# Kernel tuning notes

Measured on AMD Instinct MI355X. Metric: run time of the kernel, lower is better.

Reference implementation:

```python
import jax, jax.numpy as jnp
import numpy as np

N_NODES, T, C_IN, B = 207, 12, 4, 4
NT = N_NODES * T
D, H = 96, 4
HD = D // H
FF = 4 * D
ENC_L, DEC_L = 4, 1
N_MASK = int(NT * 0.75)
N_UNMASK = NT - N_MASK
MAX_NEIGH = 40
ATTN_SCALE = 1.0 / float(np.sqrt(HD))
SQRT_D = float(np.sqrt(D))


def _ln(x, g, b, eps=1e-5):
    m = jnp.mean(x, -1, keepdims=True)
    v = jnp.mean((x - m) ** 2, -1, keepdims=True)
    return (x - m) * jax.lax.rsqrt(v + eps) * g + b


def _transformer(x, attn_mask, layers):
    # x: [B, S, D]; attn_mask: [S, S] bool (True = disallowed) or None.
    x = x * SQRT_D  # nn.Transformer-style input scaling
    def step(h, p):
        aw, ab, W1, B1, W2, B2, LN = p
        Bq, S, _ = h.shape
        q = (h @ aw[0] + ab[0]).reshape(Bq, S, H, HD)
        k = (h @ aw[1] + ab[1]).reshape(Bq, S, H, HD)
        v = (h @ aw[2] + ab[2]).reshape(Bq, S, H, HD)
        scores = jnp.einsum('bqhd,bkhd->bhqk', q, k) * ATTN_SCALE
        if attn_mask is not None:
            scores = jnp.where(attn_mask, jnp.float32(-1e30), scores)
        probs = jax.nn.softmax(scores, axis=-1)
        o = jnp.einsum('bhqk,bkhd->bqhd', probs, v).reshape(Bq, S, D)
        h = _ln(h + o @ aw[3] + ab[3], LN[0, 0], LN[0, 1])  # post-norm (torch default)
        f = jax.nn.relu(h @ W1 + B1) @ W2 + B2
        h = _ln(h + f, LN[1, 0], LN[1, 1])
        return h, None
    x, _ = jax.lax.scan(step, x, layers)
    return x


def _layer_params(key, nlayers):
    ks = jax.random.split(key, 3)
    attn_w = jax.random.normal(ks[0], (nlayers, 4, D, D), jnp.float32) / float(np.sqrt(D))
    w1 = jax.random.normal(ks[1], (nlayers, D, FF), jnp.float32) / float(np.sqrt(D))
    w2 = jax.random.normal(ks[2], (nlayers, FF, D), jnp.float32) / float(np.sqrt(FF))
    ln = jnp.broadcast_to(jnp.stack([jnp.ones(D), jnp.zeros(D)]), (nlayers, 2, 2, D)).astype(jnp.float32)
    return (attn_w, jnp.zeros((nlayers, 4, D), jnp.float32), w1,
            jnp.zeros((nlayers, FF), jnp.float32), w2, jnp.zeros((nlayers, D), jnp.float32), ln)


def setup_inputs() -> dict:
    key = jax.random.key(0)
    ks = jax.random.split(key, 12)
    rng = np.random.default_rng(42)
    perm = rng.permutation(NT)
    masked_idx = jnp.asarray(np.sort(perm[:N_MASK]), jnp.int32)
    unmasked_idx = jnp.asarray(np.sort(perm[N_MASK:]), jnp.int32)
    ea = _layer_params(ks[3], ENC_L)
    da = _layer_params(ks[4], DEC_L)
    return dict(
        history_data=jax.random.uniform(ks[0], (B, T, N_NODES, C_IN), jnp.float32),
        unmasked_idx=unmasked_idx, masked_idx=masked_idx,
        nodevec1=jax.random.normal(ks[1], (N_NODES, 10), jnp.float32),
        nodevec2=jax.random.normal(ks[2], (10, N_NODES), jnp.float32),
        dim_w=jax.random.normal(ks[5], (1, D), jnp.float32),
        dim_b=jnp.zeros((D,), jnp.float32),
        pos_emb=jax.random.uniform(ks[6], (NT, D), jnp.float32, -0.02, 0.02),
        tod_w=jax.random.normal(ks[7], (1, D), jnp.float32) * 0.02,
        tod_b=jnp.zeros((D,), jnp.float32),
        dow_w=jax.random.normal(ks[8], (1, D), jnp.float32) * 0.02,
        dow_b=jnp.zeros((D,), jnp.float32),
        mask_token=jax.random.normal(ks[9], (D,), jnp.float32) * 0.02,
        enc_attn_w=ea[0], enc_attn_b=ea[1], enc_ffn_w1=ea[2], enc_ffn_b1=ea[3],
        enc_ffn_w2=ea[4], enc_ffn_b2=ea[5], enc_ln=ea[6],
        enc_norm_g=jnp.ones((D,), jnp.float32), enc_norm_b=jnp.zeros((D,), jnp.float32),
        e2d_w=jax.random.normal(ks[10], (D, D), jnp.float32) / float(np.sqrt(D)),
        e2d_b=jnp.zeros((D,), jnp.float32),
        dec_attn_w=da[0], dec_attn_b=da[1], dec_ffn_w1=da[2], dec_ffn_b1=da[3],
        dec_ffn_w2=da[4], dec_ffn_b2=da[5], dec_ln=da[6],
        dec_norm_g=jnp.ones((D,), jnp.float32), dec_norm_b=jnp.zeros((D,), jnp.float32),
        out_w=jax.random.normal(ks[11], (D, 1), jnp.float32) / float(np.sqrt(D)),
        out_b=jnp.zeros((1,), jnp.float32),
    )


def reference(history_data, unmasked_idx, masked_idx, nodevec1, nodevec2,
              dim_w, dim_b, pos_emb, tod_w, tod_b, dow_w, dow_b, mask_token,
              enc_attn_w, enc_attn_b, enc_ffn_w1, enc_ffn_b1, enc_ffn_w2, enc_ffn_b2, enc_ln,
              enc_norm_g, enc_norm_b, e2d_w, e2d_b,
              dec_attn_w, dec_attn_b, dec_ffn_w1, dec_ffn_b1, dec_ffn_w2, dec_ffn_b2, dec_ln,
              dec_norm_g, dec_norm_b, out_w, out_b):
    hist = jnp.transpose(history_data, (0, 2, 3, 1))  # [B, N, C, T]
    tod = hist[:, :, 3:4, :].reshape(B, NT, 1)
    dow = hist[:, :, 2:3, :].reshape(B, NT, 1)
    # --- adaptive graph: softmax(relu(v1 v2)), threshold + top-40, straight-through ---
    A = jax.nn.softmax(jax.nn.relu(nodevec1 @ nodevec2), axis=1)
    kth = -jnp.sort(-A, axis=1)[:, MAX_NEIGH:MAX_NEIGH + 1]  # (MAX_NEIGH+1)-th largest per row
    keep = jnp.logical_and(A > 1.0 / N_NODES, A > kth).astype(A.dtype)
    bin_mask = jax.lax.stop_gradient(keep - A) + A
    adpA = A * bin_mask
    adpA_full = jnp.repeat(jnp.repeat(adpA, T, axis=0), T, axis=1)  # [NT, NT] block structure
    # --- embed + positional/temporal encoding ---
    x = jnp.transpose(hist[:, :, 0:1, :], (0, 1, 3, 2)) @ dim_w + dim_b  # [B, N, T, D]
    token = x.reshape(B, NT, D) + pos_emb + (tod @ tod_w + tod_b) + (dow @ dow_w + dow_b)
    # --- encoder over unmasked tokens with graph-derived attention mask ---
    enc_in = token[:, unmasked_idx, :]
    A_sub = adpA_full[unmasked_idx][:, unmasked_idx]
    attn_mask = A_sub == 0  # ~A.bool(): True = disallowed
    h = _transformer(enc_in, attn_mask,
                     (enc_attn_w, enc_attn_b, enc_ffn_w1, enc_ffn_b1, enc_ffn_w2, enc_ffn_b2, enc_ln))
    h = _ln(h, enc_norm_g, enc_norm_b)
    # --- decoder ---
    h = h @ e2d_w + e2d_b
    h_masked = (mask_token[None, None, :] + pos_emb[masked_idx]
                + (tod[:, masked_idx] @ tod_w + tod_b)
                + (dow[:, masked_idx] @ dow_w + dow_b))  # [B, N_MASK, D]
    full = jnp.concatenate([h, h_masked], axis=1)  # [B, NT, D]
    full = _transformer(full, None,
                        (dec_attn_w, dec_attn_b, dec_ffn_w1, dec_ffn_b1, dec_ffn_w2, dec_ffn_b2, dec_ln))
    full = _ln(full, dec_norm_g, dec_norm_b)
    recon = full @ out_w + out_b  # [B, NT, 1]
    recon_masked = recon[:, N_UNMASK:, :]
    label = jnp.transpose(hist, (0, 1, 3, 2))[:, :, :, 0].reshape(B, NT, 1)
    label_masked = label[:, masked_idx, :]
    return recon_masked, label_masked
```

## Files before the change

### kernel.cpp

```cpp
#include <hip/hip_runtime.h>
#include <math.h>

#define N_NODES 207
#define T_STEPS 12
#define NT 2484
#define BQ 4
#define DIM 96
#define NH 4
#define HD 24
#define FFD 384
#define N_MASK 1863
#define N_UNMASK 621
#define MAX_NEIGH 40
#define ATTN_SCALE 0.20412414523193154f
#define SQRT_DF 9.797958971132712f
#define KT 256
#define NMW 20

static inline int cdiv(int a, int b) { return (a + b - 1) / b; }

__global__ __launch_bounds__(256) void adj_kernel(const float* __restrict__ nv1,
                                                  const float* __restrict__ nv2,
                                                  float* __restrict__ keep) {
    int r = blockIdx.x, t = threadIdx.x;
    __shared__ float a[N_NODES];
    __shared__ float red[256];
    __shared__ int   redi[256];
    __shared__ int   taken[N_NODES];
    __shared__ float v1[10];
    __shared__ float kth;
    if (t < 10) v1[t] = nv1[r * 10 + t];
    __syncthreads();
    if (t < N_NODES) {
        float s = 0.f;
#pragma unroll
        for (int c = 0; c < 10; ++c) s += v1[c] * nv2[c * N_NODES + t];
        a[t] = fmaxf(s, 0.f);
        taken[t] = 0;
    }
    __syncthreads();
    red[t] = (t < N_NODES) ? a[t] : -3e38f;
    __syncthreads();
    for (int s = 128; s > 0; s >>= 1) {
        if (t < s) red[t] = fmaxf(red[t], red[t + s]);
        __syncthreads();
    }
    float mx = red[0];
    __syncthreads();
    float e = 0.f;
    if (t < N_NODES) e = __expf(a[t] - mx);
    red[t] = e;
    __syncthreads();
    for (int s = 128; s > 0; s >>= 1) {
        if (t < s) red[t] += red[t + s];
        __syncthreads();
    }
    float inv = 1.f / red[0];
    __syncthreads();
    if (t < N_NODES) a[t] = e * inv;
    __syncthreads();
    for (int round = 0; round <= MAX_NEIGH; ++round) {
        red[t]  = (t < N_NODES && !taken[t]) ? a[t] : -1.f;
        redi[t] = t;
        __syncthreads();
        for (int s = 128; s > 0; s >>= 1) {
            if (t < s && red[t + s] > red[t]) { red[t] = red[t + s]; redi[t] = redi[t + s]; }
            __syncthreads();
        }
        if (t == 0) {
            taken[redi[0]] = 1;
            if (round == MAX_NEIGH) kth = red[0];
        }
        __syncthreads();
    }
    if (t < N_NODES) {
        float av = a[t];
        keep[r * N_NODES + t] = (av > (1.f / 207.f) && av > kth) ? 1.f : 0.f;
    }
}

__global__ void unnode_kernel(const int* __restrict__ uidx, int* __restrict__ unn) {
    int i = blockIdx.x * blockDim.x + threadIdx.x;
    if (i < N_UNMASK) unn[i] = uidx[i] / T_STEPS;
}

__global__ void maskbits_kernel(const float* __restrict__ keep, const int* __restrict__ unn,
                                unsigned int* __restrict__ mw) {
    int q = blockIdx.x;
    int w = threadIdx.x;
    if (w >= NMW) return;
    const float* krow = keep + unn[q] * N_NODES;
    unsigned int word = 0;
    for (int j = 0; j < 32; ++j) {
        int k = w * 32 + j;
        if (k < N_UNMASK && krow[unn[k]] != 0.f) word |= (1u << j);
    }
    mw[q * NMW + w] = word;
}

__global__ void encin_kernel(const float* __restrict__ hist, const int* __restrict__ uidx,
                             const float* __restrict__ dim_w, const float* __restrict__ dim_b,
                             const float* __restrict__ pos,
                             const float* __restrict__ tod_w, const float* __restrict__ tod_b,
                             const float* __restrict__ dow_w, const float* __restrict__ dow_b,
                             float* __restrict__ h) {
    int idx = blockIdx.x * blockDim.x + threadIdx.x;
    if (idx >= BQ * N_UNMASK * DIM) return;
    int d = idx % DIM;
    int q = (idx / DIM) % N_UNMASK;
    int b = idx / (DIM * N_UNMASK);
    int u = uidx[q];
    int n = u / T_STEPS, t = u % T_STEPS;
    const float* hp = hist + ((size_t)(b * T_STEPS + t) * N_NODES + n) * 4;
    float h0 = hp[0], dw = hp[2], td = hp[3];
    float val = h0 * dim_w[d] + dim_b[d] + pos[u * DIM + d]
              + td * tod_w[d] + tod_b[d] + dw * dow_w[d] + dow_b[d];
    h[idx] = val * SQRT_DF;
}

__global__ void hmasked_kernel(const float* __restrict__ hist, const int* __restrict__ midx,
                               const float* __restrict__ mask_token, const float* __restrict__ pos,
                               const float* __restrict__ tod_w, const float* __restrict__ tod_b,
                               const float* __restrict__ dow_w, const float* __restrict__ dow_b,
                               float* __restrict__ full) {
    int idx = blockIdx.x * blockDim.x + threadIdx.x;
    if (idx >= BQ * N_MASK * DIM) return;
    int d = idx % DIM;
    int j = (idx / DIM) % N_MASK;
    int b = idx / (DIM * N_MASK);
    int m = midx[j];
    int n = m / T_STEPS, t = m % T_STEPS;
    const float* hp = hist + ((size_t)(b * T_STEPS + t) * N_NODES + n) * 4;
    float dw = hp[2], td = hp[3];
    float val = mask_token[d] + pos[m * DIM + d]
              + td * tod_w[d] + tod_b[d] + dw * dow_w[d] + dow_b[d];
    full[((size_t)(b * NT) + N_UNMASK + j) * DIM + d] = val * SQRT_DF;
}

__global__ void label_kernel(const float* __restrict__ hist, const int* __restrict__ midx,
                             float* __restrict__ out) {
    int idx = blockIdx.x * blockDim.x + threadIdx.x;
    if (idx >= BQ * N_MASK) return;
    int j = idx % N_MASK;
    int b = idx / N_MASK;
    int m = midx[j];
    int n = m / T_STEPS, t = m % T_STEPS;
    out[BQ * N_MASK + idx] = hist[((size_t)(b * T_STEPS + t) * N_NODES + n) * 4 + 0];
}

#define ACCROW(accv, av)                                          \
    accv.x += av.x*w0.x + av.y*w1.x + av.z*w2.x + av.w*w3.x;      \
    accv.y += av.x*w0.y + av.y*w1.y + av.z*w2.y + av.w*w3.y;      \
    accv.z += av.x*w0.z + av.y*w1.z + av.z*w2.z + av.w*w3.z;      \
    accv.w += av.x*w0.w + av.y*w1.w + av.z*w2.w + av.w*w3.w;

template<int WMODE>
__global__ __launch_bounds__(256) void tgemm_kernel(const float* __restrict__ A,
                                                    const float* __restrict__ W,
                                                    const float* __restrict__ bias,
                                                    const float* __restrict__ res,
                                                    float* __restrict__ C,
                                                    int M, int N, int K, int gm,
                                                    int relu, float scale, int rmode) {
    __shared__ float As[64][100];
    __shared__ float Ws[96][64];
    int tid = threadIdx.x;
    int bm = blockIdx.x % gm;
    int bn = blockIdx.x / gm;
    int m0 = bm * 64, n0 = bn * 64;
    int tn4 = (tid & 15) * 4;
    int tm4 = (tid >> 4) * 4;
    float4 acc0 = {0,0,0,0}, acc1 = {0,0,0,0}, acc2 = {0,0,0,0}, acc3 = {0,0,0,0};

    for (int kc = 0; kc < K; kc += 96) {
        if (kc) __syncthreads();
#pragma unroll
        for (int i = 0; i < 6; ++i) {
            int f = i * 256 + tid;
            int r = f / 24, c4 = (f % 24) * 4;
            float4 v = {0,0,0,0};
            if (m0 + r < M) v = *(const float4*)(A + (size_t)(m0 + r) * K + kc + c4);
            *(float4*)&As[r][c4] = v;
        }
#pragma unroll
        for (int i = 0; i < 6; ++i) {
            int f = i * 256 + tid;
            int kr = f >> 4, n4 = (f & 15) * 4;
            int gn = n0 + n4;
            float4 v = {0,0,0,0};
            if (gn < N) {
                if (WMODE == 0) {
                    v = *(const float4*)(W + (size_t)(kc + kr) * N + gn);
                } else {
                    int gg = gn / 96, nc = gn - gg * 96;
                    v = *(const float4*)(W + (size_t)gg * 9216 + (kc + kr) * 96 + nc);
                }
            }
            *(float4*)&Ws[kr][n4] = v;
        }
        __syncthreads();
#pragma unroll 4
        for (int k = 0; k < 96; k += 4) {
            float4 a0 = *(const float4*)&As[tm4 + 0][k];
            float4 a1 = *(const float4*)&As[tm4 + 1][k];
            float4 a2 = *(const float4*)&As[tm4 + 2][k];
            float4 a3 = *(const float4*)&As[tm4 + 3][k];
            float4 w0 = *(const float4*)&Ws[k + 0][tn4];
            float4 w1 = *(const float4*)&Ws[k + 1][tn4];
            float4 w2 = *(const float4*)&Ws[k + 2][tn4];
            float4 w3 = *(const float4*)&Ws[k + 3][tn4];
            ACCROW(acc0, a0)
            ACCROW(acc1, a1)
            ACCROW(acc2, a2)
            ACCROW(acc3, a3)
        }
    }

    int gn = n0 + tn4;
    if (gn >= N) return;
    float4 bv = *(const float4*)(bias + gn);
    float4 av[4] = {acc0, acc1, acc2, acc3};
#pragma unroll
    for (int i = 0; i < 4; ++i) {
        int grow = m0 + tm4 + i;
        if (grow >= M) break;
        float4 acc = av[i];
        acc.x += bv.x; acc.y += bv.y; acc.z += bv.z; acc.w += bv.w;
        if (res) {
            int rr = grow;
            if (rmode) { int bb = grow / N_MASK; rr = bb * NT + N_UNMASK + (grow - bb * N_MASK); }
            float4 rv = *(const float4*)(res + (size_t)rr * N + gn);
            acc.x += rv.x; acc.y += rv.y; acc.z += rv.z; acc.w += rv.w;
        }
        if (relu) {
            acc.x = fmaxf(acc.x, 0.f); acc.y = fmaxf(acc.y, 0.f);
            acc.z = fmaxf(acc.z, 0.f); acc.w = fmaxf(acc.w, 0.f);
        }
        acc.x *= scale; acc.y *= scale; acc.z *= scale; acc.w *= scale;
        *(float4*)(C + (size_t)grow * N + gn) = acc;
    }
}

template<int QPL>
__global__ __launch_bounds__(256) void fattn_kernel(const float* __restrict__ Qp,
                                                    const float* __restrict__ Kp,
                                                    const float* __restrict__ Vp,
                                                    float* __restrict__ Pm,
                                                    float* __restrict__ Pl,
                                                    float* __restrict__ Pacc,
                                                    const unsigned int* __restrict__ maskw,
                                                    int S, int Sq, int qoff,
                                                    int nqt, int NS, int rs) {
    __shared__ float smem[12288];
    float* Ks = smem;
    float* Vs = smem + 6144;

    int t = threadIdx.x;
    int w = t >> 6, lane = t & 63;
    int bid = blockIdx.x;
    int ns = bid % NS; int r1 = bid / NS;
    int qt = r1 % nqt; r1 /= nqt;
    int hh = r1 % NH;
    int b  = r1 / NH;

    float qr[QPL][HD];
    bool qvalid[QPL];
#pragma unroll
    for (int h = 0; h < QPL; ++h) {
        int qidx = qt * (64 * QPL) + h * 64 + lane;
        qvalid[h] = qidx < Sq;
        if (qvalid[h]) {
            const float* qp = Qp + ((size_t)(b * S + qoff + qidx)) * rs + hh * HD;
#pragma unroll
            for (int i = 0; i < 6; ++i) {
                float4 v = *(const float4*)(qp + i * 4);
                qr[h][i*4+0] = v.x; qr[h][i*4+1] = v.y;
                qr[h][i*4+2] = v.z; qr[h][i*4+3] = v.w;
            }
        } else {
#pragma unroll
            for (int d = 0; d < HD; ++d) qr[h][d] = 0.f;
        }
    }

    float m[QPL], l[QPL];
    float acc[QPL][HD];
#pragma unroll
    for (int h = 0; h < QPL; ++h) {
        m[h] = -1e30f; l[h] = 0.f;
#pragma unroll
        for (int d = 0; d < HD; ++d) acc[h][d] = 0.f;
    }

    int ntile = (S + KT - 1) / KT;
    int tpn = (ntile + NS - 1) / NS;
    int c0 = ns * tpn;
    int c1 = min(c0 + tpn, ntile);

    for (int c = c0; c < c1; ++c) {
        __syncthreads();
        int base_k = c * KT;
#pragma unroll
        for (int i = 0; i < 6; ++i) {
            int fi = i * 256 + t;
            int row = fi / 6, cc = fi - row * 6;
            int gk = base_k + row;
            float4 kv = {0,0,0,0};
            float4 vv = {0,0,0,0};
            if (gk < S) {
                size_t roff = ((size_t)(b * S + gk)) * rs + hh * HD + cc * 4;
                kv = *(const float4*)(Kp + roff);
                vv = *(const float4*)(Vp + roff);
            }
            *(float4*)(Ks + row * HD + cc * 4) = kv;
            *(float4*)(Vs + row * HD + cc * 4) = vv;
        }
        __syncthreads();

        unsigned int mw0 = ~0u, mw1 = ~0u;
        if (QPL == 1 && maskw) {
            int qidx = qt * 64 + lane;
            if (qidx < Sq) {
                int wi = c * 8 + w * 2;
                mw0 = (wi     < NMW) ? maskw[qidx * NMW + wi]     : 0u;
                mw1 = (wi + 1 < NMW) ? maskw[qidx * NMW + wi + 1] : 0u;
            }
        }

        for (int g = 0; g < 16; ++g) {
            float sgrp[QPL][4];
            float pv[QPL][4];
#pragma unroll
            for (int j = 0; j < 4; ++j) {
                int j2 = g * 4 + j;
                int kk = (w << 6) + j2;
                int gk = base_k + kk;
                const float4* kr = (const float4*)(Ks + kk * HD);
                float d0[QPL];
#pragma unroll
                for (int h = 0; h < QPL; ++h) d0[h] = 0.f;
#pragma unroll
                for (int i = 0; i < 6; ++i) {
                    float4 kv = kr[i];
#pragma unroll
                    for (int h = 0; h < QPL; ++h) {
                        d0[h] += qr[h][i*4+0]*kv.x + qr[h][i*4+1]*kv.y
                               + qr[h][i*4+2]*kv.z + qr[h][i*4+3]*kv.w;
                    }
                }
#pragma unroll
                for (int h = 0; h < QPL; ++h) {
                    float s = d0[h] * ATTN_SCALE;
                    if (QPL == 1 && maskw) {
                        unsigned int wsel = (j2 & 32) ? mw1 : mw0;
                        if (!((wsel >> (j2 & 31)) & 1u)) s = -1e30f;
                    }
                    if (gk >= S) s = -INFINITY;
                    sgrp[h][j] = s;
                }
            }
#pragma unroll
            for (int h = 0; h < QPL; ++h) {
                float gmx = fmaxf(fmaxf(sgrp[h][0], sgrp[h][1]),
                                  fmaxf(sgrp[h][2], sgrp[h][3]));
                if (gmx > m[h]) {
                    float f = __expf(m[h] - gmx);
                    l[h] *= f;
#pragma unroll
                    for (int d = 0; d < HD; ++d) acc[h][d] *= f;
                    m[h] = gmx;
                }
#pragma unroll
                for (int j = 0; j < 4; ++j) {
                    float p = __expf(sgrp[h][j] - m[h]);
                    pv[h][j] = p;
                    l[h] += p;
                }
            }
#pragma unroll
            for (int j = 0; j < 4; ++j) {
                int kk = (w << 6) + g * 4 + j;
                const float4* vr = (const float4*)(Vs + kk * HD);
#pragma unroll
                for (int i = 0; i < 6; ++i) {
                    float4 vv = vr[i];
#pragma unroll
                    for (int h = 0; h < QPL; ++h) {
                        acc[h][i*4+0] += pv[h][j]*vv.x;
                        acc[h][i*4+1] += pv[h][j]*vv.y;
                        acc[h][i*4+2] += pv[h][j]*vv.z;
                        acc[h][i*4+3] += pv[h][j]*vv.w;
                    }
                }
            }
        }
    }

#pragma unroll
    for (int h = 0; h < QPL; ++h) {
        __syncthreads();
        float* my = smem + (size_t)(w * 64 + lane) * 27;
        my[0] = m[h]; my[1] = l[h];
#pragma unroll
        for (int d = 0; d < HD; ++d) my[2 + d] = acc[h][d];
        __syncthreads();
        if (t < 64) {
            int qidx = qt * (64 * QPL) + h * 64 + t;
            if (qidx < Sq) {
                float M2 = -INFINITY;
#pragma unroll
                for (int w2 = 0; w2 < 4; ++w2)
                    M2 = fmaxf(M2, smem[(size_t)(w2 * 64 + t) * 27]);
                float L = 0.f;
                float o[HD];
#pragma unroll
                for (int d = 0; d < HD; ++d) o[d] = 0.f;
#pragma unroll
                for (int w2 = 0; w2 < 4; ++w2) {
                    const float* pp = smem + (size_t)(w2 * 64 + t) * 27;
                    float f = __expf(pp[0] - M2);
                    L += pp[1] * f;
#pragma unroll
                    for (int d = 0; d < HD; ++d) o[d] += pp[2 + d] * f;
                }
                size_t pb = ((size_t)((b * NH + hh) * NS + ns)) * Sq + qidx;
                Pm[pb] = M2;
                Pl[pb] = L;
                float* pa = Pacc + pb * 24;
#pragma unroll
                for (int i = 0; i < 6; ++i)
                    *(float4*)(pa + i * 4) = make_float4(o[i*4+0], o[i*4+1],
                                                         o[i*4+2], o[i*4+3]);
            }
        }
    }
}

__global__ __launch_bounds__(256) void attn_combine_kernel(const float* __restrict__ Pm,
                                                           const float* __restrict__ Pl,
                                                           const float* __restrict__ Pacc,
                                                           float* __restrict__ O,
                                                           int Sq, int NS) {
    int tid = blockIdx.x * 256 + threadIdx.x;
    if (tid >= BQ * NH * Sq * 6) return;
    int d4 = tid % 6;
    int q  = (tid / 6) % Sq;
    int bh = tid / (6 * Sq);
    float M = -1e30f;
    for (int ns = 0; ns < NS; ++ns)
        M = fmaxf(M, Pm[((size_t)bh * NS + ns) * Sq + q]);
    float L = 0.f;
    float ax = 0.f, ay = 0.f, az = 0.f, aw = 0.f;
    for (int ns = 0; ns < NS; ++ns) {
        size_t pb = ((size_t)bh * NS + ns) * Sq + q;
        float wgt = __expf(Pm[pb] - M);
        L += wgt * Pl[pb];
        float4 f0 = *(const float4*)(Pacc + pb * 24 + d4 * 4);
        ax += wgt * f0.x; ay += wgt * f0.y;
        az += wgt * f0.z; aw += wgt * f0.w;
    }
    float inv = 1.f / L;
    int b = bh >> 2, hh = bh & 3;
    float* op = O + ((size_t)(b * Sq + q)) * DIM + hh * HD + d4 * 4;
    *(float4*)op = make_float4(ax * inv, ay * inv, az * inv, aw * inv);
}

__global__ __launch_bounds__(256) void ln_kernel(const float* __restrict__ X,
                                                 const float* __restrict__ g,
                                                 const float* __restrict__ bta,
                                                 float* __restrict__ Y, int M) {
    int row = blockIdx.x * 4 + (threadIdx.x >> 6);
    if (row >= M) return;
    int lane = threadIdx.x & 63;
    const float* x = X + (size_t)row * DIM;
    float x0 = x[lane];
    float x1 = (lane < 32) ? x[64 + lane] : 0.f;
    float s = x0 + x1;
#pragma unroll
    for (int o = 32; o; o >>= 1) s += __shfl_xor(s, o);
    float mean = s * (1.f / DIM);
    float d0 = x0 - mean;
    float d1 = (lane < 32) ? (x1 - mean) : 0.f;
    float v = d0 * d0 + d1 * d1;
#pragma unroll
    for (int o = 32; o; o >>= 1) v += __shfl_xor(v, o);
    float rs = rsqrtf(v * (1.f / DIM) + 1e-5f);
    float* y = Y + (size_t)row * DIM;
    y[lane] = d0 * rs * g[lane] + bta[lane];
    if (lane < 32) y[64 + lane] = d1 * rs * g[64 + lane] + bta[64 + lane];
}

__global__ __launch_bounds__(256) void tail_kernel(const float* __restrict__ X,
                                                   const float* __restrict__ g1,
                                                   const float* __restrict__ b1,
                                                   const float* __restrict__ g2,
                                                   const float* __restrict__ b2,
                                                   const float* __restrict__ ow,
                                                   const float* __restrict__ ob,
                                                   float* __restrict__ out, int Mtail) {
    int row = blockIdx.x * 4 + (threadIdx.x >> 6);
    if (row >= Mtail) return;
    int lane = threadIdx.x & 63;
    bool lo = lane < 32;
    const float* x = X + (size_t)row * DIM;
    float x0 = x[lane];
    float x1 = lo ? x[64 + lane] : 0.f;
    float s = x0 + x1;
#pragma unroll
    for (int o = 32; o; o >>= 1) s += __shfl_xor(s, o);
    float mean = s * (1.f / DIM);
    float d0 = x0 - mean;
    float d1 = lo ? (x1 - mean) : 0.f;
    float v = d0 * d0 + d1 * d1;
#pragma unroll
    for (int o = 32; o; o >>= 1) v += __shfl_xor(v, o);
    float rs = rsqrtf(v * (1.f / DIM) + 1e-5f);
    float y0 = d0 * rs * g1[lane] + b1[lane];
    float y1 = lo ? (d1 * rs * g1[64 + lane] + b1[64 + lane]) : 0.f;
    s = y0 + y1;
#pragma unroll
    for (int o = 32; o; o >>= 1) s += __shfl_xor(s, o);
    mean = s * (1.f / DIM);
    d0 = y0 - mean;
    d1 = lo ? (y1 - mean) : 0.f;
    v = d0 * d0 + d1 * d1;
#pragma unroll
    for (int o = 32; o; o >>= 1) v += __shfl_xor(v, o);
    rs = rsqrtf(v * (1.f / DIM) + 1e-5f);
    float z0 = d0 * rs * g2[lane] + b2[lane];
    float z1 = lo ? (d1 * rs * g2[64 + lane] + b2[64 + lane]) : 0.f;
    float a = z0 * ow[lane] + (lo ? z1 * ow[64 + lane] : 0.f);
#pragma unroll
    for (int o = 32; o; o >>= 1) a += __shfl_xor(a, o);
    if (lane == 0) out[row] = a + ob[0];
}

__global__ void copy_enc_kernel(const float* __restrict__ src, float* __restrict__ full) {
    int idx = blockIdx.x * blockDim.x + threadIdx.x;
    if (idx >= BQ * N_UNMASK * DIM) return;
    int d = idx % DIM;
    int q = (idx / DIM) % N_UNMASK;
    int b = idx / (DIM * N_UNMASK);
    full[((size_t)(b * NT) + q) * DIM + d] = src[idx];
}

extern "C" void kernel_launch(void* const* d_in, const int* in_sizes, int n_in,
                              void* d_out, int out_size, void* d_ws, size_t ws_size,
                              hipStream_t stream) {
    const float* hist   = (const float*)d_in[0];
    const int*   uidx   = (const int*)d_in[1];
    const int*   midx   = (const int*)d_in[2];
    const float* nv1    = (const float*)d_in[3];
    const float* nv2    = (const float*)d_in[4];
    const float* dim_w  = (const float*)d_in[5];
    const float* dim_b  = (const float*)d_in[6];
    const float* pos    = (const float*)d_in[7];
    const float* tod_w  = (const float*)d_in[8];
    const float* tod_b  = (const float*)d_in[9];
    const float* dow_w  = (const float*)d_in[10];
    const float* dow_b  = (const float*)d_in[11];
    const float* mtok   = (const float*)d_in[12];
    const float* eaw    = (const float*)d_in[13];
    const float* eab    = (const float*)d_in[14];
    const float* ew1    = (const float*)d_in[15];
    const float* eb1    = (const float*)d_in[16];
    const float* ew2    = (const float*)d_in[17];
    const float* eb2    = (const float*)d_in[18];
    const float* eln    = (const float*)d_in[19];
    const float* eng    = (const float*)d_in[20];
    const float* enb    = (const float*)d_in[21];
    const float* e2dw   = (const float*)d_in[22];
    const float* e2db   = (const float*)d_in[23];
    const float* daw    = (const float*)d_in[24];
    const float* dab    = (const float*)d_in[25];
    const float* dw1    = (const float*)d_in[26];
    const float* db1    = (const float*)d_in[27];
    const float* dw2    = (const float*)d_in[28];
    const float* db2    = (const float*)d_in[29];
    const float* dln    = (const float*)d_in[30];
    const float* dng    = (const float*)d_in[31];
    const float* dnb    = (const float*)d_in[32];
    const float* ow     = (const float*)d_in[33];
    const float* ob     = (const float*)d_in[34];

    float* ws = (float*)d_ws;
    float*        keep  = ws;
    int*          unn   = (int*)(ws + 43008);
    unsigned int* maskw = (unsigned int*)(ws + 44032);
    float* eh = ws + 56576;
    float* e1 = ws + 295040;
    float* e2 = ws + 1248896;
    float* et = ws + 1487360;
    float* fh = ws + 1725824;
    float* qf = ws + 2679680;
    float* dh = ws + 5541248;
    float* dt = ws + 6256640;
    float* PaccE = ws + 5541248;
    float* PmE   = ws + 6256640;
    float* PlE   = ws + 6286448;
    float* PaccD = ws + 56576;
    float* PmD   = ws + 1487360;
    float* PlD   = ws + 1546976;
    float* dLN = e1;

    float* outp = (float*)d_out;
    const int ME = BQ * N_UNMASK;
    const int MD = BQ * NT;
    const int MT = BQ * N_MASK;
    const int gmE = cdiv(ME, 64);
    const int gmD = cdiv(MD, 64);
    const int gmT = cdiv(MT, 64);
    const int NSE = 3, NSD = 2;
    const int nqtE = 10;
    const int nqtD = 15;

    adj_kernel<<<N_NODES, 256, 0, stream>>>(nv1, nv2, keep);
    unnode_kernel<<<cdiv(N_UNMASK, 256), 256, 0, stream>>>(uidx, unn);
    maskbits_kernel<<<N_UNMASK, 32, 0, stream>>>(keep, unn, maskw);
    encin_kernel<<<cdiv(ME * DIM, 256), 256, 0, stream>>>(
        hist, uidx, dim_w, dim_b, pos, tod_w, tod_b, dow_w, dow_b, eh);
    label_kernel<<<cdiv(MT, 256), 256, 0, stream>>>(hist, midx, outp);

    for (int l = 0; l < 4; ++l) {
        const float* aw = eaw + (size_t)l * 4 * DIM * DIM;
        const float* ab = eab + (size_t)l * 4 * DIM;
        tgemm_kernel<1><<<gmE * 5, 256, 0, stream>>>(
            eh, aw, ab, nullptr, e1, ME, 288, 96, gmE, 0, 1.f, 0);
        fattn_kernel<1><<<BQ * NH * nqtE * NSE, 256, 0, stream>>>(
            e1, e1 + 96, e1 + 192, PmE, PlE, PaccE, maskw,
            N_UNMASK, N_UNMASK, 0, nqtE, NSE, 288);
        attn_combine_kernel<<<cdiv(BQ * NH * N_UNMASK * 6, 256), 256, 0, stream>>>(
            PmE, PlE, PaccE, e2, N_UNMASK, NSE);
        tgemm_kernel<0><<<gmE * 2, 256, 0, stream>>>(
            e2, aw + 3 * DIM * DIM, ab + 3 * DIM, eh, et, ME, 96, 96, gmE, 0, 1.f, 0);
        ln_kernel<<<cdiv(ME, 4), 256, 0, stream>>>(
            et, eln + (size_t)(l * 4 + 0) * DIM, eln + (size_t)(l * 4 + 1) * DIM, eh, ME);
        tgemm_kernel<0><<<gmE * 6, 256, 0, stream>>>(
            eh, ew1 + (size_t)l * DIM * FFD, eb1 + (size_t)l * FFD, nullptr, e1,
            ME, FFD, 96, gmE, 1, 1.f, 0);
        tgemm_kernel<0><<<gmE * 2, 256, 0, stream>>>(
            e1, ew2 + (size_t)l * FFD * DIM, eb2 + (size_t)l * DIM, eh, et,
            ME, 96, FFD, gmE, 0, 1.f, 0);
        ln_kernel<<<cdiv(ME, 4), 256, 0, stream>>>(
            et, eln + (size_t)(l * 4 + 2) * DIM, eln + (size_t)(l * 4 + 3) * DIM, eh, ME);
    }
    ln_kernel<<<cdiv(ME, 4), 256, 0, stream>>>(eh, eng, enb, e2, ME);
    tgemm_kernel<0><<<gmE * 2, 256, 0, stream>>>(
        e2, e2dw, e2db, nullptr, et, ME, 96, 96, gmE, 0, SQRT_DF, 0);
    copy_enc_kernel<<<cdiv(ME * DIM, 256), 256, 0, stream>>>(et, fh);
    hmasked_kernel<<<cdiv(MT * DIM, 256), 256, 0, stream>>>(
        hist, midx, mtok, pos, tod_w, tod_b, dow_w, dow_b, fh);

    tgemm_kernel<1><<<gmD * 5, 256, 0, stream>>>(
        fh, daw, dab, nullptr, qf, MD, 288, 96, gmD, 0, 1.f, 0);
    fattn_kernel<2><<<BQ * NH * nqtD * NSD, 256, 0, stream>>>(
        qf, qf + 96, qf + 192, PmD, PlD, PaccD, nullptr,
        NT, N_MASK, N_UNMASK, nqtD, NSD, 288);
    attn_combine_kernel<<<cdiv(BQ * NH * N_MASK * 6, 256), 256, 0, stream>>>(
        PmD, PlD, PaccD, dh, N_MASK, NSD);
    tgemm_kernel<0><<<gmT * 2, 256, 0, stream>>>(
        dh, daw + 3 * DIM * DIM, dab + 3 * DIM, fh, dt, MT, 96, 96, gmT, 0, 1.f, 1);
    ln_kernel<<<cdiv(MT, 4), 256, 0, stream>>>(dt, dln + 0 * DIM, dln + 1 * DIM, dLN, MT);
    tgemm_kernel<0><<<gmT * 6, 256, 0, stream>>>(
        dLN, dw1, db1, nullptr, qf, MT, FFD, 96, gmT, 1, 1.f, 0);
    tgemm_kernel<0><<<gmT * 2, 256, 0, stream>>>(
        qf, dw2, db2, dLN, dh, MT, 96, FFD, gmT, 0, 1.f, 0);
    tail_kernel<<<cdiv(MT, 4), 256, 0, stream>>>(
        dh, dln + 2 * DIM, dln + 3 * DIM, dng, dnb, ow, ob, outp, MT);
}
```

Before: 700.4 us.

## Fuse residual add and LayerNorm into full-width N=96 GEMM epilogue

Adds a GEMM kernel where each block computes a 64-row tile across all 96 output columns, so the residual add and post-norm LayerNorm can run in the epilogue via 16-lane shuffle reductions. This replaces the separate out-projection/FFN2 GEMM plus ln_kernel launches in the encoder and decoder, and writes the encoder-to-decoder projection straight into the decoder buffer, which removes copy_enc_kernel. The tail kernel drops its first LayerNorm because that work now happens in the fused epilogue. The cost is fewer blocks per launch, one per 64 rows instead of two or more, which lowers parallelism on these small M sizes, and a larger shared-memory footprint per block.

```diff
diff --git a/kernel.cpp b/kernel.cpp
--- a/kernel.cpp
+++ b/kernel.cpp
@@ -238,6 +238,118 @@
         }
         acc.x *= scale; acc.y *= scale; acc.z *= scale; acc.w *= scale;
         *(float4*)(C + (size_t)grow * N + gn) = acc;
+    }
+}
+
+template<int DOLN>
+__global__ __launch_bounds__(256) void tgemm96_kernel(const float* __restrict__ A,
+                                                      const float* __restrict__ W,
+                                                      const float* __restrict__ bias,
+                                                      const float* __restrict__ res,
+                                                      const float* __restrict__ lng,
+                                                      const float* __restrict__ lnb,
+                                                      float* __restrict__ C,
+                                                      int M, int K,
+                                                      float scale, int rmode, int omode) {
+    __shared__ float As[64][100];
+    __shared__ float Ws[96][100];
+    int tid = threadIdx.x;
+    int m0 = blockIdx.x * 64;
+    int tc = tid & 15;
+    int tr = tid >> 4;
+    int colBase = tc * 6;
+    float acc[4][6];
+#pragma unroll
+    for (int r = 0; r < 4; ++r)
+#pragma unroll
+        for (int c = 0; c < 6; ++c) acc[r][c] = 0.f;
+
+    for (int kc = 0; kc < K; kc += 96) {
+        if (kc) __syncthreads();
+#pragma unroll
+        for (int i = 0; i < 6; ++i) {
+            int f = i * 256 + tid;
+            int r = f / 24, c4 = (f % 24) * 4;
+            float4 v = {0,0,0,0};
+            if (m0 + r < M) v = *(const float4*)(A + (size_t)(m0 + r) * K + kc + c4);
+            *(float4*)&As[r][c4] = v;
+        }
+#pragma unroll
+        for (int i = 0; i < 9; ++i) {
+            int f = i * 256 + tid;
+            int kr = f / 24, c4 = (f % 24) * 4;
+            float4 v = *(const float4*)(W + (size_t)(kc + kr) * 96 + c4);
+            *(float4*)&Ws[kr][c4] = v;
+        }
+        __syncthreads();
+#pragma unroll 4
+        for (int k = 0; k < 96; k += 4) {
+            float4 a0 = *(const float4*)&As[tr * 4 + 0][k];
+            float4 a1 = *(const float4*)&As[tr * 4 + 1][k];
+            float4 a2 = *(const float4*)&As[tr * 4 + 2][k];
+            float4 a3 = *(const float4*)&As[tr * 4 + 3][k];
+#pragma unroll
+            for (int i = 0; i < 4; ++i) {
+                float2 w01 = *(const float2*)&Ws[k + i][colBase];
+                float2 w23 = *(const float2*)&Ws[k + i][colBase + 2];
+                float2 w45 = *(const float2*)&Ws[k + i][colBase + 4];
+                float wv[6] = {w01.x, w01.y, w23.x, w23.y, w45.x, w45.y};
+                float ai[4] = { (i==0?a0.x:(i==1?a0.y:(i==2?a0.z:a0.w))),
+                                (i==0?a1.x:(i==1?a1.y:(i==2?a1.z:a1.w))),
+                                (i==0?a2.x:(i==1?a2.y:(i==2?a2.z:a2.w))),
+                                (i==0?a3.x:(i==1?a3.y:(i==2?a3.z:a3.w))) };
+#pragma unroll
+                for (int r = 0; r < 4; ++r)
+#pragma unroll
+                    for (int c = 0; c < 6; ++c)
+                        acc[r][c] += ai[r] * wv[c];
+            }
+        }
+    }
+
+    float bv[6];
+#pragma unroll
+    for (int c = 0; c < 6; ++c) bv[c] = bias[colBase + c];
+
+#pragma unroll
+    for (int r = 0; r < 4; ++r) {
+        int grow = m0 + tr * 4 + r;
+        bool valid = grow < M;
+        float v[6];
+#pragma unroll
+        for (int c = 0; c < 6; ++c) v[c] = acc[r][c] + bv[c];
+        if (res && valid) {
+            int rr = grow;
+            if (rmode) { int bb = grow / N_MASK; rr = bb * NT + N_UNMASK + (grow - bb * N_MASK); }
+            const float* rp = res + (size_t)rr * 96 + colBase;
+#pragma unroll
+            for (int c = 0; c < 6; ++c) v[c] += rp[c];
+        }
+#pragma unroll
+        for (int c = 0; c < 6; ++c) v[c] *= scale;
+        if (DOLN) {
+            float s = ((v[0] + v[1]) + (v[2] + v[3])) + (v[4] + v[5]);
+#pragma unroll
+            for (int o = 1; o <= 8; o <<= 1) s += __shfl_xor(s, o);
+            float mean = s * (1.f / 96.f);
+            float var = 0.f;
+#pragma unroll
+            for (int c = 0; c < 6; ++c) { float d = v[c] - mean; var += d * d; }
+#pragma unroll
+            for (int o = 1; o <= 8; o <<= 1) var += __shfl_xor(var, o);
+            float rs = rsqrtf(var * (1.f / 96.f) + 1e-5f);
+#pragma unroll
+            for (int c = 0; c < 6; ++c)
+                v[c] = (v[c] - mean) * rs * lng[colBase + c] + lnb[colBase + c];
+        }
+        if (valid) {
+            int orow = grow;
+            if (omode) { int bb = grow / N_UNMASK; orow = bb * NT + (grow - bb * N_UNMASK); }
+            float* cp = C + (size_t)orow * 96 + colBase;
+            *(float2*)(cp)     = make_float2(v[0], v[1]);
+            *(float2*)(cp + 2) = make_float2(v[2], v[3]);
+            *(float2*)(cp + 4) = make_float2(v[4], v[5]);
+        }
     }
 }
 
@@ -491,8 +603,6 @@
 }
 
 __global__ __launch_bounds__(256) void tail_kernel(const float* __restrict__ X,
-                                                   const float* __restrict__ g1,
-                                                   const float* __restrict__ b1,
                                                    const float* __restrict__ g2,
                                                    const float* __restrict__ b2,
                                                    const float* __restrict__ ow,
@@ -503,45 +613,24 @@
     int lane = threadIdx.x & 63;
     bool lo = lane < 32;
     const float* x = X + (size_t)row * DIM;
-    float x0 = x[lane];
-    float x1 = lo ? x[64 + lane] : 0.f;
-    float s = x0 + x1;
+    float y0 = x[lane];
+    float y1 = lo ? x[64 + lane] : 0.f;
+    float s = y0 + y1;
 #pragma unroll
     for (int o = 32; o; o >>= 1) s += __shfl_xor(s, o);
     float mean = s * (1.f / DIM);
-    float d0 = x0 - mean;
-    float d1 = lo ? (x1 - mean) : 0.f;
+    float d0 = y0 - mean;
+    float d1 = lo ? (y1 - mean) : 0.f;
     float v = d0 * d0 + d1 * d1;
 #pragma unroll
     for (int o = 32; o; o >>= 1) v += __shfl_xor(v, o);
     float rs = rsqrtf(v * (1.f / DIM) + 1e-5f);
-    float y0 = d0 * rs * g1[lane] + b1[lane];
-    float y1 = lo ? (d1 * rs * g1[64 + lane] + b1[64 + lane]) : 0.f;
-    s = y0 + y1;
-#pragma unroll
-    for (int o = 32; o; o >>= 1) s += __shfl_xor(s, o);
-    mean = s * (1.f / DIM);
-    d0 = y0 - mean;
-    d1 = lo ? (y1 - mean) : 0.f;
-    v = d0 * d0 + d1 * d1;
-#pragma unroll
-    for (int o = 32; o; o >>= 1) v += __shfl_xor(v, o);
-    rs = rsqrtf(v * (1.f / DIM) + 1e-5f);
     float z0 = d0 * rs * g2[lane] + b2[lane];
     float z1 = lo ? (d1 * rs * g2[64 + lane] + b2[64 + lane]) : 0.f;
     float a = z0 * ow[lane] + (lo ? z1 * ow[64 + lane] : 0.f);
 #pragma unroll
     for (int o = 32; o; o >>= 1) a += __shfl_xor(a, o);
     if (lane == 0) out[row] = a + ob[0];
-}
-
-__global__ void copy_enc_kernel(const float* __restrict__ src, float* __restrict__ full) {
-    int idx = blockIdx.x * blockDim.x + threadIdx.x;
-    if (idx >= BQ * N_UNMASK * DIM) return;
-    int d = idx % DIM;
-    int q = (idx / DIM) % N_UNMASK;
-    int b = idx / (DIM * N_UNMASK);
-    full[((size_t)(b * NT) + q) * DIM + d] = src[idx];
 }
 
 extern "C" void kernel_launch(void* const* d_in, const int* in_sizes, int n_in,
@@ -590,7 +679,6 @@
     float* eh = ws + 56576;
     float* e1 = ws + 295040;
     float* e2 = ws + 1248896;
-    float* et = ws + 1487360;
     float* fh = ws + 1725824;
     float* qf = ws + 2679680;
     float* dh = ws + 5541248;
@@ -601,7 +689,6 @@
     float* PaccD = ws + 56576;
     float* PmD   = ws + 1487360;
     float* PlD   = ws + 1546976;
-    float* dLN = e1;
 
     float* outp = (float*)d_out;
     const int ME = BQ * N_UNMASK;
@@ -631,23 +718,21 @@
             N_UNMASK, N_UNMASK, 0, nqtE, NSE, 288);
         attn_combine_kernel<<<cdiv(BQ * NH * N_UNMASK * 6, 256), 256, 0, stream>>>(
             PmE, PlE, PaccE, e2, N_UNMASK, NSE);
-        tgemm_kernel<0><<<gmE * 2, 256, 0, stream>>>(
-            e2, aw + 3 * DIM * DIM, ab + 3 * DIM, eh, et, ME, 96, 96, gmE, 0, 1.f, 0);
-        ln_kernel<<<cdiv(ME, 4), 256, 0, stream>>>(
-            et, eln + (size_t)(l * 4 + 0) * DIM, eln + (size_t)(l * 4 + 1) * DIM, eh, ME);
+        tgemm96_kernel<1><<<gmE, 256, 0, stream>>>(
+            e2, aw + 3 * DIM * DIM, ab + 3 * DIM, eh,
+            eln + (size_t)(l * 4 + 0) * DIM, eln + (size_t)(l * 4 + 1) * DIM,
+            eh, ME, 96, 1.f, 0, 0);
         tgemm_kernel<0><<<gmE * 6, 256, 0, stream>>>(
             eh, ew1 + (size_t)l * DIM * FFD, eb1 + (size_t)l * FFD, nullptr, e1,
             ME, FFD, 96, gmE, 1, 1.f, 0);
-        tgemm_kernel<0><<<gmE * 2, 256, 0, stream>>>(
-            e1, ew2 + (size_t)l * FFD * DIM, eb2 + (size_t)l * DIM, eh, et,
-            ME, 96, FFD, gmE, 0, 1.f, 0);
-        ln_kernel<<<cdiv(ME, 4), 256, 0, stream>>>(
-            et, eln + (size_t)(l * 4 + 2) * DIM, eln + (size_t)(l * 4 + 3) * DIM, eh, ME);
+        tgemm96_kernel<1><<<gmE, 256, 0, stream>>>(
+            e1, ew2 + (size_t)l * FFD * DIM, eb2 + (size_t)l * DIM, eh,
+            eln + (size_t)(l * 4 + 2) * DIM, eln + (size_t)(l * 4 + 3) * DIM,
+            eh, ME, FFD, 1.f, 0, 0);
     }
     ln_kernel<<<cdiv(ME, 4), 256, 0, stream>>>(eh, eng, enb, e2, ME);
-    tgemm_kernel<0><<<gmE * 2, 256, 0, stream>>>(
-        e2, e2dw, e2db, nullptr, et, ME, 96, 96, gmE, 0, SQRT_DF, 0);
-    copy_enc_kernel<<<cdiv(ME * DIM, 256), 256, 0, stream>>>(et, fh);
+    tgemm96_kernel<0><<<gmE, 256, 0, stream>>>(
+        e2, e2dw, e2db, nullptr, nullptr, nullptr, fh, ME, 96, SQRT_DF, 0, 1);
     hmasked_kernel<<<cdiv(MT * DIM, 256), 256, 0, stream>>>(
         hist, midx, mtok, pos, tod_w, tod_b, dow_w, dow_b, fh);
 
@@ -658,13 +743,13 @@
         NT, N_MASK, N_UNMASK, nqtD, NSD, 288);
     attn_combine_kernel<<<cdiv(BQ * NH * N_MASK * 6, 256), 256, 0, stream>>>(
         PmD, PlD, PaccD, dh, N_MASK, NSD);
-    tgemm_kernel<0><<<gmT * 2, 256, 0, stream>>>(
-        dh, daw + 3 * DIM * DIM, dab + 3 * DIM, fh, dt, MT, 96, 96, gmT, 0, 1.f, 1);
-    ln_kernel<<<cdiv(MT, 4), 256, 0, stream>>>(dt, dln + 0 * DIM, dln + 1 * DIM, dLN, MT);
+    tgemm96_kernel<1><<<gmT, 256, 0, stream>>>(
+        dh, daw + 3 * DIM * DIM, dab + 3 * DIM, fh,
+        dln + 0 * DIM, dln + 1 * DIM, dt, MT, 96, 1.f, 1, 0);
     tgemm_kernel<0><<<gmT * 6, 256, 0, stream>>>(
-        dLN, dw1, db1, nullptr, qf, MT, FFD, 96, gmT, 1, 1.f, 0);
-    tgemm_kernel<0><<<gmT * 2, 256, 0, stream>>>(
-        qf, dw2, db2, dLN, dh, MT, 96, FFD, gmT, 0, 1.f, 0);
+        dt, dw1, db1, nullptr, qf, MT, FFD, 96, gmT, 1, 1.f, 0);
+    tgemm96_kernel<1><<<gmT, 256, 0, stream>>>(
+        qf, dw2, db2, dt, dln + 2 * DIM, dln + 3 * DIM, dh, MT, FFD, 1.f, 0, 0);
     tail_kernel<<<cdiv(MT, 4), 256, 0, stream>>>(
-        dh, dln + 2 * DIM, dln + 3 * DIM, dng, dnb, ow, ob, outp, MT);
-}
+        dh, dng, dnb, ow, ob, outp, MT);
+}
```

Measured after the change: 715.1 us. 1.02x slower.

## Fuse post-FFN LayerNorm into next GEMM prologue and swizzle attention blocks by XCD

Applied to the files above, without the earlier changes.

The second LayerNorm of each encoder layer is folded into the A-tile load of the next layer's QKV GEMM, which writes the normalized rows back for the residual path. The final encoder norm is applied as a second LN pass inside the encoder-to-decoder projection. Both remove standalone ln_kernel launches and their global round trips. The unnode kernel is also folded into maskbits, and attention blocks are remapped so each batch-head lands on one XCD for L2 locality. The cost is redundant LN work in every N-tile block and extra barriers in the GEMM prologue.

```diff
diff --git a/kernel.cpp b/kernel.cpp
--- a/kernel.cpp
+++ b/kernel.cpp
@@ -16,6 +16,7 @@
 #define SQRT_DF 9.797958971132712f
 #define KT 256
 #define NMW 20
+#define NBH 16
 
 static inline int cdiv(int a, int b) { return (a + b - 1) / b; }
 
@@ -79,21 +80,16 @@
     }
 }
 
-__global__ void unnode_kernel(const int* __restrict__ uidx, int* __restrict__ unn) {
-    int i = blockIdx.x * blockDim.x + threadIdx.x;
-    if (i < N_UNMASK) unn[i] = uidx[i] / T_STEPS;
-}
-
-__global__ void maskbits_kernel(const float* __restrict__ keep, const int* __restrict__ unn,
+__global__ void maskbits_kernel(const float* __restrict__ keep, const int* __restrict__ uidx,
                                 unsigned int* __restrict__ mw) {
     int q = blockIdx.x;
     int w = threadIdx.x;
     if (w >= NMW) return;
-    const float* krow = keep + unn[q] * N_NODES;
+    const float* krow = keep + (uidx[q] / T_STEPS) * N_NODES;
     unsigned int word = 0;
     for (int j = 0; j < 32; ++j) {
         int k = w * 32 + j;
-        if (k < N_UNMASK && krow[unn[k]] != 0.f) word |= (1u << j);
+        if (k < N_UNMASK && krow[uidx[k] / T_STEPS] != 0.f) word |= (1u << j);
     }
     mw[q * NMW + w] = word;
 }
@@ -154,16 +150,23 @@
     accv.z += av.x*w0.z + av.y*w1.z + av.z*w2.z + av.w*w3.z;      \
     accv.w += av.x*w0.w + av.y*w1.w + av.z*w2.w + av.w*w3.w;
 
-template<int WMODE>
+template<int WMODE, int LNA>
 __global__ __launch_bounds__(256) void tgemm_kernel(const float* __restrict__ A,
                                                     const float* __restrict__ W,
                                                     const float* __restrict__ bias,
                                                     const float* __restrict__ res,
                                                     float* __restrict__ C,
                                                     int M, int N, int K, int gm,
-                                                    int relu, float scale, int rmode) {
+                                                    int relu, float scale, int rmode,
+                                                    const float* __restrict__ g1,
+                                                    const float* __restrict__ b1,
+                                                    const float* __restrict__ g2,
+                                                    const float* __restrict__ b2,
+                                                    float* __restrict__ wb) {
     __shared__ float As[64][100];
     __shared__ float Ws[96][64];
+    __shared__ float lred[64][4];
+    __shared__ float lmv[64][2];
     int tid = threadIdx.x;
     int bm = blockIdx.x % gm;
     int bn = blockIdx.x / gm;
@@ -199,6 +202,56 @@
             *(float4*)&Ws[kr][n4] = v;
         }
         __syncthreads();
+
+        if (LNA > 0 && kc == 0) {
+#pragma unroll
+            for (int pass = 0; pass < LNA; ++pass) {
+                const float* lg = pass ? g2 : g1;
+                const float* lb = pass ? b2 : b1;
+                int row = tid >> 2, part = tid & 3;
+                float s = 0.f;
+                for (int c = part * 24; c < part * 24 + 24; ++c) s += As[row][c];
+                lred[row][part] = s;
+                __syncthreads();
+                float mean = (lred[row][0] + lred[row][1] + lred[row][2] + lred[row][3]) * (1.f / 96.f);
+                float s2 = 0.f;
+                for (int c = part * 24; c < part * 24 + 24; ++c) {
+                    float d = As[row][c] - mean; s2 += d * d;
+                }
+                __syncthreads();
+                lred[row][part] = s2;
+                __syncthreads();
+                if (part == 0) {
+                    float var = (lred[row][0] + lred[row][1] + lred[row][2] + lred[row][3]) * (1.f / 96.f);
+                    lmv[row][0] = mean;
+                    lmv[row][1] = rsqrtf(var + 1e-5f);
+                }
+                __syncthreads();
+#pragma unroll
+                for (int i = 0; i < 6; ++i) {
+                    int f = i * 256 + tid;
+                    int r = f / 24, c4 = (f % 24) * 4;
+                    float mn = lmv[r][0], rsd = lmv[r][1];
+                    float4 v = *(float4*)&As[r][c4];
+                    v.x = (v.x - mn) * rsd * lg[c4 + 0] + lb[c4 + 0];
+                    v.y = (v.y - mn) * rsd * lg[c4 + 1] + lb[c4 + 1];
+                    v.z = (v.z - mn) * rsd * lg[c4 + 2] + lb[c4 + 2];
+                    v.w = (v.w - mn) * rsd * lg[c4 + 3] + lb[c4 + 3];
+                    *(float4*)&As[r][c4] = v;
+                }
+                __syncthreads();
+            }
+            if (wb && bn == 0) {
+#pragma unroll
+                for (int i = 0; i < 6; ++i) {
+                    int f = i * 256 + tid;
+                    int r = f / 24, c4 = (f % 24) * 4;
+                    if (m0 + r < M)
+                        *(float4*)(wb + (size_t)(m0 + r) * 96 + c4) = *(const float4*)&As[r][c4];
+                }
+            }
+        }
+
 #pragma unroll 4
         for (int k = 0; k < 96; k += 4) {
             float4 a0 = *(const float4*)&As[tm4 + 0][k];
@@ -249,6 +302,7 @@
                                                     float* __restrict__ Pl,
                                                     float* __restrict__ Pacc,
                                                     const unsigned int* __restrict__ maskw,
+                                                    int swz,
                                                     int S, int Sq, int qoff,
                                                     int nqt, int NS, int rs) {
     __shared__ float smem[12288];
@@ -258,10 +312,19 @@
     int t = threadIdx.x;
     int w = t >> 6, lane = t & 63;
     int bid = blockIdx.x;
-    int ns = bid % NS; int r1 = bid / NS;
-    int qt = r1 % nqt; r1 /= nqt;
-    int hh = r1 % NH;
-    int b  = r1 / NH;
+    int ns, qt, hh, b;
+    if (swz) {
+        int xcd = bid & 7, slot = bid >> 3;
+        int spb = nqt * NS;
+        int bh = xcd + 8 * (slot / spb);
+        int r = slot % spb;
+        qt = r / NS; ns = r % NS;
+        b = bh >> 2; hh = bh & 3;
+    } else {
+        ns = bid % NS; int r1 = bid / NS;
+        qt = r1 % nqt; r1 /= nqt;
+        hh = r1 % NH; b = r1 / NH;
+    }
 
     float qr[QPL][HD];
     bool qvalid[QPL];
@@ -442,7 +505,7 @@
                                                            float* __restrict__ O,
                                                            int Sq, int NS) {
     int tid = blockIdx.x * 256 + threadIdx.x;
-    if (tid >= BQ * NH * Sq * 6) return;
+    if (tid >= NBH * Sq * 6) return;
     int d4 = tid % 6;
     int q  = (tid / 6) % Sq;
     int bh = tid / (6 * Sq);
@@ -585,7 +648,6 @@
 
     float* ws = (float*)d_ws;
     float*        keep  = ws;
-    int*          unn   = (int*)(ws + 43008);
     unsigned int* maskw = (unsigned int*)(ws + 44032);
     float* eh = ws + 56576;
     float* e1 = ws + 295040;
@@ -601,7 +663,7 @@
     float* PaccD = ws + 56576;
     float* PmD   = ws + 1487360;
     float* PlD   = ws + 1546976;
-    float* dLN = e1;
+    float* dLN   = e1;
 
     float* outp = (float*)d_out;
     const int ME = BQ * N_UNMASK;
@@ -615,8 +677,7 @@
     const int nqtD = 15;
 
     adj_kernel<<<N_NODES, 256, 0, stream>>>(nv1, nv2, keep);
-    unnode_kernel<<<cdiv(N_UNMASK, 256), 256, 0, stream>>>(uidx, unn);
-    maskbits_kernel<<<N_UNMASK, 32, 0, stream>>>(keep, unn, maskw);
+    maskbits_kernel<<<N_UNMASK, 32, 0, stream>>>(keep, uidx, maskw);
     encin_kernel<<<cdiv(ME * DIM, 256), 256, 0, stream>>>(
         hist, uidx, dim_w, dim_b, pos, tod_w, tod_b, dow_w, dow_b, eh);
     label_kernel<<<cdiv(MT, 256), 256, 0, stream>>>(hist, midx, outp);
@@ -624,47 +685,62 @@
     for (int l = 0; l < 4; ++l) {
         const float* aw = eaw + (size_t)l * 4 * DIM * DIM;
         const float* ab = eab + (size_t)l * 4 * DIM;
-        tgemm_kernel<1><<<gmE * 5, 256, 0, stream>>>(
-            eh, aw, ab, nullptr, e1, ME, 288, 96, gmE, 0, 1.f, 0);
-        fattn_kernel<1><<<BQ * NH * nqtE * NSE, 256, 0, stream>>>(
-            e1, e1 + 96, e1 + 192, PmE, PlE, PaccE, maskw,
+        if (l == 0) {
+            tgemm_kernel<1,0><<<gmE * 5, 256, 0, stream>>>(
+                eh, aw, ab, nullptr, e1, ME, 288, 96, gmE, 0, 1.f, 0,
+                nullptr, nullptr, nullptr, nullptr, nullptr);
+        } else {
+            tgemm_kernel<1,1><<<gmE * 5, 256, 0, stream>>>(
+                et, aw, ab, nullptr, e1, ME, 288, 96, gmE, 0, 1.f, 0,
+                eln + (size_t)((l - 1) * 4 + 2) * DIM,
+                eln + (size_t)((l - 1) * 4 + 3) * DIM,
+                nullptr, nullptr, eh);
+        }
+        fattn_kernel<1><<<NBH * nqtE * NSE, 256, 0, stream>>>(
+            e1, e1 + 96, e1 + 192, PmE, PlE, PaccE, maskw, 1,
             N_UNMASK, N_UNMASK, 0, nqtE, NSE, 288);
-        attn_combine_kernel<<<cdiv(BQ * NH * N_UNMASK * 6, 256), 256, 0, stream>>>(
+        attn_combine_kernel<<<cdiv(NBH * N_UNMASK * 6, 256), 256, 0, stream>>>(
             PmE, PlE, PaccE, e2, N_UNMASK, NSE);
-        tgemm_kernel<0><<<gmE * 2, 256, 0, stream>>>(
-            e2, aw + 3 * DIM * DIM, ab + 3 * DIM, eh, et, ME, 96, 96, gmE, 0, 1.f, 0);
+        tgemm_kernel<0,0><<<gmE * 2, 256, 0, stream>>>(
+            e2, aw + 3 * DIM * DIM, ab + 3 * DIM, eh, et, ME, 96, 96, gmE, 0, 1.f, 0,
+            nullptr, nullptr, nullptr, nullptr, nullptr);
         ln_kernel<<<cdiv(ME, 4), 256, 0, stream>>>(
             et, eln + (size_t)(l * 4 + 0) * DIM, eln + (size_t)(l * 4 + 1) * DIM, eh, ME);
-        tgemm_kernel<0><<<gmE * 6, 256, 0, stream>>>(
+        tgemm_kernel<0,0><<<gmE * 6, 256, 0, stream>>>(
             eh, ew1 + (size_t)l * DIM * FFD, eb1 + (size_t)l * FFD, nullptr, e1,
-            ME, FFD, 96, gmE, 1, 1.f, 0);
-        tgemm_kernel<0><<<gmE * 2, 256, 0, stream>>>(
+            ME, FFD, 96, gmE, 1, 1.f, 0,
+            nullptr, nullptr, nullptr, nullptr, nullptr);
+        tgemm_kernel<0,0><<<gmE * 2, 256, 0, stream>>>(
             e1, ew2 + (size_t)l * FFD * DIM, eb2 + (size_t)l * DIM, eh, et,
-            ME, 96, FFD, gmE, 0, 1.f, 0);
-        ln_kernel<<<cdiv(ME, 4), 256, 0, stream>>>(
-            et, eln + (size_t)(l * 4 + 2) * DIM, eln + (size_t)(l * 4 + 3) * DIM, eh, ME);
-    }
-    ln_kernel<<<cdiv(ME, 4), 256, 0, stream>>>(eh, eng, enb, e2, ME);
-    tgemm_kernel<0><<<gmE * 2, 256, 0, stream>>>(
-        e2, e2dw, e2db, nullptr, et, ME, 96, 96, gmE, 0, SQRT_DF, 0);
-    copy_enc_kernel<<<cdiv(ME * DIM, 256), 256, 0, stream>>>(et, fh);
+            ME, 96, FFD, gmE, 0, 1.f, 0,
+            nullptr, nullptr, nullptr, nullptr, nullptr);
+    }
+    tgemm_kernel<0,2><<<gmE * 2, 256, 0, stream>>>(
+        et, e2dw, e2db, nullptr, e2, ME, 96, 96, gmE, 0, SQRT_DF, 0,
+        eln + (size_t)(3 * 4 + 2) * DIM, eln + (size_t)(3 * 4 + 3) * DIM,
+        eng, enb, nullptr);
+    copy_enc_kernel<<<cdiv(ME * DIM, 256), 256, 0, stream>>>(e2, fh);
     hmasked_kernel<<<cdiv(MT * DIM, 256), 256, 0, stream>>>(
         hist, midx, mtok, pos, tod_w, tod_b, dow_w, dow_b, fh);
 
-    tgemm_kernel<1><<<gmD * 5, 256, 0, stream>>>(
-        fh, daw, dab, nullptr, qf, MD, 288, 96, gmD, 0, 1.f, 0);
-    fattn_kernel<2><<<BQ * NH * nqtD * NSD, 256, 0, stream>>>(
-        qf, qf + 96, qf + 192, PmD, PlD, PaccD, nullptr,
+    tgemm_kernel<1,0><<<gmD * 5, 256, 0, stream>>>(
+        fh, daw, dab, nullptr, qf, MD, 288, 96, gmD, 0, 1.f, 0,
+        nullptr, nullptr, nullptr, nullptr, nullptr);
+    fattn_kernel<2><<<NBH * nqtD * NSD, 256, 0, stream>>>(
+        qf, qf + 96, qf + 192, PmD, PlD, PaccD, nullptr, 1,
         NT, N_MASK, N_UNMASK, nqtD, NSD, 288);
-    attn_combine_kernel<<<cdiv(BQ * NH * N_MASK * 6, 256), 256, 0, stream>>>(
+    attn_combine_kernel<<<cdiv(NBH * N_MASK * 6, 256), 256, 0, stream>>>(
         PmD, PlD, PaccD, dh, N_MASK, NSD);
-    tgemm_kernel<0><<<gmT * 2, 256, 0, stream>>>(
-        dh, daw + 3 * DIM * DIM, dab + 3 * DIM, fh, dt, MT, 96, 96, gmT, 0, 1.f, 1);
+    tgemm_kernel<0,0><<<gmT * 2, 256, 0, stream>>>(
+        dh, daw + 3 * DIM * DIM, dab + 3 * DIM, fh, dt, MT, 96, 96, gmT, 0, 1.f, 1,
+        nullptr, nullptr, nullptr, nullptr, nullptr);
     ln_kernel<<<cdiv(MT, 4), 256, 0, stream>>>(dt, dln + 0 * DIM, dln + 1 * DIM, dLN, MT);
-    tgemm_kernel<0><<<gmT * 6, 256, 0, stream>>>(
-        dLN, dw1, db1, nullptr, qf, MT, FFD, 96, gmT, 1, 1.f, 0);
-    tgemm_kernel<0><<<gmT * 2, 256, 0, stream>>>(
-        qf, dw2, db2, dLN, dh, MT, 96, FFD, gmT, 0, 1.f, 0);
+    tgemm_kernel<0,0><<<gmT * 6, 256, 0, stream>>>(
+        dLN, dw1, db1, nullptr, qf, MT, FFD, 96, gmT, 1, 1.f, 0,
+        nullptr, nullptr, nullptr, nullptr, nullptr);
+    tgemm_kernel<0,0><<<gmT * 2, 256, 0, stream>>>(
+        qf, dw2, db2, dLN, dh, MT, 96, FFD, gmT, 0, 1.f, 0,
+        nullptr, nullptr, nullptr, nullptr, nullptr);
     tail_kernel<<<cdiv(MT, 4), 256, 0, stream>>>(
         dh, dln + 2 * DIM, dln + 3 * DIM, dng, dnb, ow, ob, outp, MT);
 }
```

Result: no change. 688.2 us (-1.7%).
